# Optimization experiments

Measured on AMD Instinct MI355X. Metric: run time of the kernel, lower is better.

The kernel has to match this reference:

```python
import jax, jax.numpy as jnp
import numpy as np

NUM_HEADS = 8
D_MODEL = 512
HEAD_DIM = D_MODEL // NUM_HEADS
LN_EPS = 1e-5


def setup_inputs() -> dict:
    key = jax.random.key(0)
    ks = jax.random.split(key, 12)
    B, S = 8, 1024
    P = 2 * S - 1  # relative position length
    s = 0.02
    return {
        "x": jax.random.normal(ks[0], (B, S, D_MODEL), jnp.float32),
        "pos_emb": jax.random.normal(ks[1], (P, D_MODEL), jnp.float32),
        "ln_w": jnp.ones((D_MODEL,), jnp.float32),
        "ln_b": jnp.zeros((D_MODEL,), jnp.float32),
        "Wq": jax.random.normal(ks[2], (D_MODEL, D_MODEL), jnp.float32) * s,
        "bq": jax.random.normal(ks[3], (D_MODEL,), jnp.float32) * s,
        "Wk": jax.random.normal(ks[4], (D_MODEL, D_MODEL), jnp.float32) * s,
        "bk": jax.random.normal(ks[5], (D_MODEL,), jnp.float32) * s,
        "Wv": jax.random.normal(ks[6], (D_MODEL, D_MODEL), jnp.float32) * s,
        "bv": jax.random.normal(ks[7], (D_MODEL,), jnp.float32) * s,
        "Wo": jax.random.normal(ks[8], (D_MODEL, D_MODEL), jnp.float32) * s,
        "bo": jax.random.normal(ks[9], (D_MODEL,), jnp.float32) * s,
        "Wp": jax.random.normal(ks[10], (D_MODEL, D_MODEL), jnp.float32) * s,
        "pos_bias_u": jax.random.normal(ks[11], (D_MODEL,), jnp.float32) * s,
        "pos_bias_v": jax.random.normal(jax.random.fold_in(key, 99), (D_MODEL,), jnp.float32) * s,
    }


def _rel_shift(x):
    # x: [B, H, S, P] -> Transformer-XL relative shift, return [B, H, S, S]
    b, h, s, p = x.shape
    x = jnp.pad(x, ((0, 0), (0, 0), (0, 0), (1, 0)))  # pad one zero column on left
    x = x.reshape(b, h, p + 1, s)[:, :, 1:, :]
    x = x.reshape(b, h, s, p)
    return x[:, :, :, :s]


def reference(x, pos_emb, ln_w, ln_b, Wq, bq, Wk, bk, Wv, bv, Wo, bo, Wp,
              pos_bias_u, pos_bias_v):
    B, S, D = x.shape
    H, hd = NUM_HEADS, HEAD_DIM
    # LayerNorm
    mu = jnp.mean(x, axis=-1, keepdims=True)
    var = jnp.mean(jnp.square(x - mu), axis=-1, keepdims=True)
    h_ = (x - mu) * jax.lax.rsqrt(var + LN_EPS) * ln_w + ln_b
    # Projections (torch Linear: y = x @ W.T + b)
    q = (h_ @ Wq.T + bq).reshape(B, S, H, hd).transpose(0, 2, 1, 3)  # [B,H,S,hd]
    k = (h_ @ Wk.T + bk).reshape(B, S, H, hd).transpose(0, 2, 1, 3)
    v = (h_ @ Wv.T + bv).reshape(B, S, H, hd).transpose(0, 2, 1, 3)
    bias_u = pos_bias_u.reshape(1, H, 1, hd)
    bias_v = pos_bias_v.reshape(1, H, 1, hd)
    content = jnp.einsum('bhqd,bhkd->bhqk', q + bias_u, k)
    # Positional projection: [P, D] -> [H, P, hd]
    p = (pos_emb @ Wp.T).reshape(-1, H, hd).transpose(1, 0, 2)
    pos_score = jnp.einsum('bhqd,hpd->bhqp', q + bias_v, p)
    pos_score = _rel_shift(pos_score)
    scale = 1.0 / np.sqrt(hd).astype(np.float32)
    attn = jax.nn.softmax((content + pos_score) * scale, axis=-1)
    out = jnp.einsum('bhqk,bhkd->bhqd', attn, v)
    out = out.transpose(0, 2, 1, 3).reshape(B, S, D)
    out = out @ Wo.T + bo
    return x + out
```

## Files before the change

### kernel.cpp

```cpp
#include <hip/hip_runtime.h>
#include <hip/hip_bf16.h>


typedef __attribute__((ext_vector_type(8))) short  s16x8;
typedef __attribute__((ext_vector_type(8))) __bf16 bfv8;
typedef __attribute__((ext_vector_type(4))) float  f32x4;
typedef __attribute__((ext_vector_type(4))) unsigned u32x4;

__device__ __forceinline__ float b2f(short s){
  unsigned u = ((unsigned)(unsigned short)s) << 16;
  float f; __builtin_memcpy(&f, &u, 4); return f;
}
__device__ __forceinline__ short f2b(float f){
  unsigned u; __builtin_memcpy(&u, &f, 4);
  u = (u + 0x7fffu + ((u >> 16) & 1u)) >> 16;
  return (short)u;
}
__device__ __forceinline__ unsigned pk2(float lo, float hi){
  __hip_bfloat162 t = __float22bfloat162_rn(make_float2(lo, hi));
  unsigned u; __builtin_memcpy(&u, &t, 4); return u;
}
__device__ __forceinline__ f32x4 MFMA(s16x8 a, s16x8 b, f32x4 c){
  return __builtin_amdgcn_mfma_f32_16x16x32_bf16(
      __builtin_bit_cast(bfv8, a), __builtin_bit_cast(bfv8, b), c, 0, 0, 0);
}
__device__ __forceinline__ void gload_lds16(const void* g, void* l){
  __builtin_amdgcn_global_load_lds(
      (const __attribute__((address_space(1))) void*)g,
      (__attribute__((address_space(3))) void*)l, 16, 0, 0);
}
__device__ __forceinline__ void cvt8(const float* in, short* out, size_t i8){
  f32x4 a = *(const f32x4*)(in + i8*8);
  f32x4 b = *(const f32x4*)(in + i8*8 + 4);
  u32x4 o;
  o[0] = pk2(a[0],a[1]); o[1] = pk2(a[2],a[3]);
  o[2] = pk2(b[0],b[1]); o[3] = pk2(b[2],b[3]);
  *(u32x4*)(out + i8*8) = o;
}

__global__ __launch_bounds__(256) void prep_kernel(
    const float* __restrict__ Wq, const float* __restrict__ Wk,
    const float* __restrict__ Wv, const float* __restrict__ Wo,
    const float* __restrict__ Wp, const float* __restrict__ pos,
    const float* __restrict__ x, const float* __restrict__ lnw, const float* __restrict__ lnb,
    short* __restrict__ wqkv, short* __restrict__ wo, short* __restrict__ wp,
    short* __restrict__ posbf, short* __restrict__ h_bf)
{
  int bid = blockIdx.x, tid = threadIdx.x;
  if(bid < 640){
    int w = bid >> 7;
    size_t i = (size_t)(bid & 127)*256 + tid;
    const float* src; short* dst;
    if(w == 0){ src = Wq; dst = wqkv; }
    else if(w == 1){ src = Wk; dst = wqkv + 262144; }
    else if(w == 2){ src = Wv; dst = wqkv + 524288; }
    else if(w == 3){ src = Wo; dst = wo; }
    else { src = Wp; dst = wp; }
    cvt8(src, dst, i);
  } else if(bid < 1152){
    size_t i = (size_t)(bid - 640)*256 + tid;
    if(i < 131008) cvt8(pos, posbf, i);
  } else {
    int row = (bid - 1152)*4 + (tid >> 6);
    int lane = tid & 63;
    const float* xr = x + (size_t)row*512;
    f32x4 v0 = *(const f32x4*)(xr + lane*8);
    f32x4 v1 = *(const f32x4*)(xr + lane*8 + 4);
    float s  = v0[0]+v0[1]+v0[2]+v0[3]+v1[0]+v1[1]+v1[2]+v1[3];
    float s2 = v0[0]*v0[0]+v0[1]*v0[1]+v0[2]*v0[2]+v0[3]*v0[3]
             + v1[0]*v1[0]+v1[1]*v1[1]+v1[2]*v1[2]+v1[3]*v1[3];
    #pragma unroll
    for(int m=1;m<64;m<<=1){ s += __shfl_xor(s,m); s2 += __shfl_xor(s2,m); }
    float mu = s * (1.0f/512.0f);
    float rs = rsqrtf(s2*(1.0f/512.0f) - mu*mu + 1e-5f);
    float y[8];
    #pragma unroll
    for(int e=0;e<8;e++){
      float xv = (e<4)? v0[e] : v1[e-4];
      int d = lane*8 + e;
      y[e] = (xv - mu)*rs*lnw[d] + lnb[d];
    }
    u32x4 o;
    o[0]=pk2(y[0],y[1]); o[1]=pk2(y[2],y[3]); o[2]=pk2(y[4],y[5]); o[3]=pk2(y[6],y[7]);
    *(u32x4*)(h_bf + (size_t)row*512 + lane*8) = o;
  }
}

__global__ __launch_bounds__(256) void gemm_fused(
    const short* __restrict__ h_bf, const short* __restrict__ wqkv,
    const float* __restrict__ bq, const float* __restrict__ bk, const float* __restrict__ bv,
    const short* __restrict__ posbf, const short* __restrict__ wp,
    short* __restrict__ q_sw, short* __restrict__ k_sw, short* __restrict__ v_sw,
    short* __restrict__ p_sw)
{
  __shared__ __align__(16) short smem[9216];
  short* At = smem;
  short* Bt = smem + 4096;
  int bid = blockIdx.x, tid = threadIdx.x;
  int wave = tid >> 6, lane = tid & 63;
  int quad = lane >> 4, l16 = lane & 15;
  int srow = lane >> 2, scol = (lane & 3)*8;
  if(bid < 768){
    int bx = bid % 12, by = bid / 12;
    int m0 = by*128, n0 = bx*128;
    int wm = wave >> 1, wn = wave & 1;
    f32x4 acc[4][4] = {};
    for(int k0=0; k0<512; k0+=32){
      #pragma unroll
      for(int c=0;c<2;c++){
        int rb = (wave + 4*c)*16;
        gload_lds16(h_bf + (size_t)(m0 + rb + srow)*512 + k0 + scol, At + rb*32);
        gload_lds16(wqkv + (size_t)(n0 + rb + srow)*512 + k0 + scol, Bt + rb*32);
      }
      __syncthreads();
      s16x8 af[4], bfr[4];
      #pragma unroll
      for(int i=0;i<4;i++) af[i]  = *(const s16x8*)(At + (wm*64 + i*16 + l16)*32 + quad*8);
      #pragma unroll
      for(int j=0;j<4;j++) bfr[j] = *(const s16x8*)(Bt + (wn*64 + j*16 + l16)*32 + quad*8);
      #pragma unroll
      for(int i=0;i<4;i++)
        #pragma unroll
        for(int j=0;j<4;j++)
          acc[i][j] = MFMA(af[i], bfr[j], acc[i][j]);
      __syncthreads();
    }
    int seg = bx >> 2;
    int nseg = (bx & 3)*128;
    int bb = by >> 3;
    const float* bsrc = (seg==0)? bq : (seg==1)? bk : bv;
    float bias_j[4];
    #pragma unroll
    for(int j=0;j<4;j++) bias_j[j] = bsrc[nseg + wn*64 + j*16 + l16];
    if(seg < 2){
      short* dst = seg ? k_sw : q_sw;
      #pragma unroll
      for(int h2=0; h2<2; h2++){
        if(wm == h2){
          #pragma unroll
          for(int i=0;i<4;i++){
            int lr = i*16 + quad*4;
            #pragma unroll
            for(int j=0;j<4;j++){
              int cl = wn*64 + j*16 + l16;
              unsigned p01 = pk2(acc[i][j][0]+bias_j[j], acc[i][j][1]+bias_j[j]);
              unsigned p23 = pk2(acc[i][j][2]+bias_j[j], acc[i][j][3]+bias_j[j]);
              smem[(lr+0)*136 + cl] = (short)p01;
              smem[(lr+1)*136 + cl] = (short)(p01>>16);
              smem[(lr+2)*136 + cl] = (short)p23;
              smem[(lr+3)*136 + cl] = (short)(p23>>16);
            }
          }
        }
        __syncthreads();
        #pragma unroll
        for(int it=0; it<4; it++){
          int ci = it*4 + wave;
          int hs = ci >> 2, tb = ci & 3;
          s16x8 vv = *(const s16x8*)(smem + (tb*16 + l16)*136 + hs*32 + quad*8);
          int hh = (nseg>>6) + (hs>>1);
          int tg = ((m0 + h2*64)>>4) + tb;
          size_t chunk = ((size_t)((bb*8 + hh)*64 + tg))*2 + (hs&1);
          *(s16x8*)(dst + chunk*512 + (size_t)lane*8) = vv;
        }
        __syncthreads();
      }
    } else {
      #pragma unroll
      for(int h2=0; h2<2; h2++){
        int jt = by*2 + h2;
        if(wm == h2){
          #pragma unroll
          for(int i=0;i<4;i++){
            int tl = i*16 + quad*4;
            #pragma unroll
            for(int j=0;j<4;j++){
              int dl = wn*64 + j*16 + l16;
              unsigned p01 = pk2(acc[i][j][0]+bias_j[j], acc[i][j][1]+bias_j[j]);
              unsigned p23 = pk2(acc[i][j][2]+bias_j[j], acc[i][j][3]+bias_j[j]);
              unsigned* w2 = (unsigned*)(smem + dl*72 + tl);
              w2[0] = p01; w2[1] = p23;
            }
          }
        }
        __syncthreads();
        #pragma unroll
        for(int it=0; it<4; it++){
          int ci = it*4 + wave;
          int hl = ci>>3, ds = (ci>>1)&3, jk = ci&1;
          s16x8 vv = *(const s16x8*)(smem + (hl*64 + ds*16 + l16)*72 + jk*32 + quad*8);
          int hh = (nseg>>6) + hl;
          size_t chunk = (((size_t)((bb*8 + hh)*16 + jt))*4 + ds)*2 + jk;
          *(s16x8*)(v_sw + chunk*512 + (size_t)lane*8) = vv;
        }
        __syncthreads();
      }
    }
  } else {
    int pid = bid - 768;
    int bx = pid % 8, by = pid / 8;
    int m0 = by*64, n0 = bx*64;
    int wm = wave >> 1, wn = wave & 1;
    f32x4 acc[2][2] = {};
    for(int k0=0; k0<512; k0+=32){
      int rb = wave*16;
      int ra = m0 + rb + srow; if(ra > 2046) ra = 2046;
      gload_lds16(posbf + (size_t)ra*512 + k0 + scol, At + rb*32);
      gload_lds16(wp + (size_t)(n0 + rb + srow)*512 + k0 + scol, Bt + rb*32);
      __syncthreads();
      s16x8 af[2], bfr[2];
      #pragma unroll
      for(int i=0;i<2;i++) af[i]  = *(const s16x8*)(At + (wm*32 + i*16 + l16)*32 + quad*8);
      #pragma unroll
      for(int j=0;j<2;j++) bfr[j] = *(const s16x8*)(Bt + (wn*32 + j*16 + l16)*32 + quad*8);
      #pragma unroll
      for(int i=0;i<2;i++)
        #pragma unroll
        for(int j=0;j<2;j++)
          acc[i][j] = MFMA(af[i], bfr[j], acc[i][j]);
      __syncthreads();
    }
    #pragma unroll
    for(int i=0;i<2;i++){
      int rowb = m0 + wm*32 + i*16 + quad*4;
      #pragma unroll
      for(int j=0;j<2;j++){
        int col = n0 + wn*32 + j*16 + l16;
        int hh = col>>6, ks = (col>>5)&1, qd = (col>>3)&3, e = col&7;
        int rblk = rowb>>4;
        size_t base = ((size_t)(((hh*128+rblk)*2+ks)*64) + qd*16)*8 + e;
        #pragma unroll
        for(int r=0;r<4;r++)
          p_sw[base + (size_t)(quad*4+r)*8] = f2b(acc[i][j][r]);
      }
    }
  }
}

__global__ __launch_bounds__(256, 3) void attn_kernel(
    const short* __restrict__ q_sw, const short* __restrict__ k_sw,
    const short* __restrict__ v_sw, const short* __restrict__ p_sw,
    const float* __restrict__ bu, const float* __restrict__ bvv,
    short* __restrict__ out)
{
  __shared__ __align__(16) short kv[2][8192];
  __shared__ __align__(16) short pwall[4608];
  int tid = threadIdx.x;
  int wave = tid >> 6, lane = tid & 63, quad = lane >> 4, l16 = lane & 15;
  int h = blockIdx.y, b = blockIdx.z, bh = b*8 + h;
  int iblk = blockIdx.x*4 + wave;
  int iw = iblk*16;
  short* pw = pwall + wave*1152;

  const short* qb = q_sw + (size_t)bh*65536;
  const short* kb = k_sw + (size_t)bh*65536;
  const short* vb = v_sw + (size_t)bh*65536;
  const short* pb = p_sw + (size_t)h*131072;

  s16x8 qu[2], qv[2];
  #pragma unroll
  for(int ks=0;ks<2;ks++){
    s16x8 qr = *(const s16x8*)(qb + ((size_t)(iblk*2+ks)*64 + lane)*8);
    short tu[8], tv[8];
    #pragma unroll
    for(int e=0;e<8;e++){
      int d = h*64 + ks*32 + quad*8 + e;
      float f = b2f(qr[e]);
      tu[e] = f2b((f + bu[d]) * 0.125f);
      tv[e] = f2b((f + bvv[d]) * 0.125f);
    }
    qu[ks] = *(s16x8*)tu; qv[ks] = *(s16x8*)tv;
  }

  s16x8 ones;
  #pragma unroll
  for(int e=0;e<8;e++) ones[e] = (short)0x3F80;

  int srcl[4]; bool lo[4];
  #pragma unroll
  for(int r=0;r<4;r++){
    int il = quad*4 + r;
    srcl[r] = quad*16 + ((l16 + 15 - il) & 15);
    lo[r]   = (l16 <= il);
  }

  f32x4 oacc[4] = {};
  f32x4 lacc = {};
  s16x8 Pa[5][2];

  auto STAGE = [&](int jt, int bufi){
    const short* base = (wave < 2) ? kb : vb;
    #pragma unroll
    for(int r=0;r<4;r++){
      int unit = wave*4 + r;
      gload_lds16(base + (size_t)jt*4096 + (unit&7)*512 + lane*8,
                  &kv[bufi][unit*512]);
    }
  };
  auto LOADPOS = [&](int jt){
    int rb0 = (jt*64 - iw + 1008) >> 4;
    #pragma unroll
    for(int nt=0;nt<5;nt++)
      #pragma unroll
      for(int ks=0;ks<2;ks++)
        Pa[nt][ks] = *(const s16x8*)(pb + (size_t)((rb0+nt)*2+ks)*512 + lane*8);
  };
  auto COMPUTE = [&](const short* Kt, const short* Vt, int next_jt){
    f32x4 ps[5];
    __builtin_amdgcn_s_setprio(1);
    #pragma unroll
    for(int nt=0;nt<5;nt++){
      f32x4 a = {};
      a = MFMA(qv[0], Pa[nt][0], a);
      a = MFMA(qv[1], Pa[nt][1], a);
      ps[nt] = a;
    }
    __builtin_amdgcn_s_setprio(0);
    if(next_jt < 16) LOADPOS(next_jt);
    float rot[4][5];
    #pragma unroll
    for(int r=0;r<4;r++)
      #pragma unroll
      for(int nt=0;nt<5;nt++) rot[r][nt] = __shfl(ps[nt][r], srcl[r]);
    #pragma unroll
    for(int js=0;js<4;js++){
      s16x8 kf0 = *(const s16x8*)(Kt + (js*2+0)*512 + lane*8);
      s16x8 kf1 = *(const s16x8*)(Kt + (js*2+1)*512 + lane*8);
      f32x4 c0;
      #pragma unroll
      for(int r=0;r<4;r++) c0[r] = lo[r] ? rot[r][js] : rot[r][js+1];
      f32x4 a = MFMA(qu[0], kf0, c0);
      a = MFMA(qu[1], kf1, a);
      int col = js*16 + l16;
      unsigned p01 = pk2(__expf(a[0]), __expf(a[1]));
      unsigned p23 = pk2(__expf(a[2]), __expf(a[3]));
      pw[(quad*4+0)*72 + col] = (short)p01;
      pw[(quad*4+1)*72 + col] = (short)(p01>>16);
      pw[(quad*4+2)*72 + col] = (short)p23;
      pw[(quad*4+3)*72 + col] = (short)(p23>>16);
    }
    __builtin_amdgcn_s_setprio(1);
    #pragma unroll
    for(int jk=0;jk<2;jk++){
      s16x8 pa = *(const s16x8*)(pw + l16*72 + jk*32 + quad*8);
      lacc = MFMA(pa, ones, lacc);
      #pragma unroll
      for(int ds=0;ds<4;ds++){
        s16x8 vf = *(const s16x8*)(Vt + (ds*2+jk)*512 + lane*8);
        oacc[ds] = MFMA(pa, vf, oacc[ds]);
      }
    }
    __builtin_amdgcn_s_setprio(0);
  };

  STAGE(0, 0);
  LOADPOS(0);
  __syncthreads();

  #pragma unroll 1
  for(int jt2=0; jt2<8; ++jt2){
    int jt = jt2*2;
    STAGE(jt+1, 1);
    COMPUTE(&kv[0][0], &kv[0][4096], jt+1);
    __syncthreads();
    if(jt2 < 7) STAGE(jt+2, 0);
    COMPUTE(&kv[1][0], &kv[1][4096], jt+2);
    __syncthreads();
  }

  float rl[4];
  #pragma unroll
  for(int r=0;r<4;r++) rl[r] = __builtin_amdgcn_rcpf(lacc[r]);
  #pragma unroll
  for(int ds=0; ds<4; ds++)
    #pragma unroll
    for(int r=0;r<4;r++)
      out[((size_t)(b*1024 + iw + quad*4 + r))*512 + h*64 + ds*16 + l16] =
          f2b(oacc[ds][r] * rl[r]);
}

__global__ __launch_bounds__(256) void gemm_out(
    const short* __restrict__ A, const short* __restrict__ B,
    const float* __restrict__ bias, const float* __restrict__ resid,
    float* __restrict__ Cout)
{
  __shared__ __align__(16) short At[64*32];
  __shared__ __align__(16) short Bt[64*32];
  int tid = threadIdx.x;
  int wave = tid >> 6, lane = tid & 63;
  int quad = lane >> 4, l16 = lane & 15;
  int wm = wave >> 1, wn = wave & 1;
  int m0 = blockIdx.y*64, n0 = blockIdx.x*64;
  int srow = lane >> 2, scol = (lane & 3)*8;
  f32x4 acc[2][2] = {};
  for(int k0=0; k0<512; k0+=32){
    int rb = wave*16;
    gload_lds16(A + (size_t)(m0 + rb + srow)*512 + k0 + scol, At + rb*32);
    gload_lds16(B + (size_t)(n0 + rb + srow)*512 + k0 + scol, Bt + rb*32);
    __syncthreads();
    s16x8 af[2], bfr[2];
    #pragma unroll
    for(int i=0;i<2;i++) af[i]  = *(const s16x8*)(At + (wm*32 + i*16 + l16)*32 + quad*8);
    #pragma unroll
    for(int j=0;j<2;j++) bfr[j] = *(const s16x8*)(Bt + (wn*32 + j*16 + l16)*32 + quad*8);
    #pragma unroll
    for(int i=0;i<2;i++)
      #pragma unroll
      for(int j=0;j<2;j++)
        acc[i][j] = MFMA(af[i], bfr[j], acc[i][j]);
    __syncthreads();
  }
  #pragma unroll
  for(int i=0;i<2;i++){
    int rowb = m0 + wm*32 + i*16 + quad*4;
    #pragma unroll
    for(int j=0;j<2;j++){
      int col = n0 + wn*32 + j*16 + l16;
      float bv = bias[col];
      #pragma unroll
      for(int r=0;r<4;r++){
        size_t idx = (size_t)(rowb + r)*512 + col;
        Cout[idx] = acc[i][j][r] + bv + resid[idx];
      }
    }
  }
}

extern "C" void kernel_launch(void* const* d_in, const int* in_sizes, int n_in,
                              void* d_out, int out_size, void* d_ws, size_t ws_size,
                              hipStream_t stream)
{
  const float* x    = (const float*)d_in[0];
  const float* pos  = (const float*)d_in[1];
  const float* lnw  = (const float*)d_in[2];
  const float* lnb  = (const float*)d_in[3];
  const float* Wq   = (const float*)d_in[4];
  const float* bq   = (const float*)d_in[5];
  const float* Wk   = (const float*)d_in[6];
  const float* bk   = (const float*)d_in[7];
  const float* Wv   = (const float*)d_in[8];
  const float* bv   = (const float*)d_in[9];
  const float* Wo   = (const float*)d_in[10];
  const float* bo   = (const float*)d_in[11];
  const float* Wp   = (const float*)d_in[12];
  const float* pbu  = (const float*)d_in[13];
  const float* pbv  = (const float*)d_in[14];
  float* out = (float*)d_out;

  char* ws = (char*)d_ws;
  short* h_bf    = (short*)(ws);
  short* q_sw    = (short*)(ws + ( 8u<<20));
  short* k_sw    = (short*)(ws + (16u<<20));
  short* v_sw    = (short*)(ws + (24u<<20));
  short* a_bf    = (short*)(ws + (32u<<20));
  short* p_sw    = (short*)(ws + (40u<<20));
  short* pos_bf  = (short*)(ws + (42u<<20));
  short* wqkv_bf = (short*)(ws + (44u<<20));
  short* wo_bf   = (short*)(ws + (47u<<20));
  short* wp_bf   = (short*)(ws + (47u<<20) + (512u<<10));

  prep_kernel<<<dim3(3200), 256, 0, stream>>>(Wq, Wk, Wv, Wo, Wp, pos,
                                              x, lnw, lnb,
                                              wqkv_bf, wo_bf, wp_bf, pos_bf, h_bf);
  gemm_fused<<<dim3(1024), 256, 0, stream>>>(h_bf, wqkv_bf, bq, bk, bv,
                                             pos_bf, wp_bf,
                                             q_sw, k_sw, v_sw, p_sw);
  attn_kernel<<<dim3(16,8,8), 256, 0, stream>>>(q_sw, k_sw, v_sw, p_sw, pbu, pbv, a_bf);
  gemm_out<<<dim3(8,128), 256, 0, stream>>>(a_bf, wo_bf, bo, x, out);
  (void)in_sizes; (void)n_in; (void)out_size; (void)ws_size;
}
```

Measured before the change: 199.0 us.

## Single-buffer V in attention, raise occupancy, remap blocks across XCDs

The attention kernel now double-buffers only K tiles and keeps a single V tile in LDS. V is loaded just-in-time for each tile, and an extra barrier is added before the PV MFMAs. This cuts LDS use so launch bounds can request 4 blocks per CU instead of 3. The grid becomes 1D with a swizzled block index that groups each (batch, head)'s query tiles onto the same XCD for K/V/P cache locality. The cost is two barriers per tile instead of one, and V loads are exposed with less overlap.

```diff
diff --git a/kernel.cpp b/kernel.cpp
--- a/kernel.cpp
+++ b/kernel.cpp
@@ -237,18 +237,22 @@
   }
 }
 
-__global__ __launch_bounds__(256, 3) void attn_kernel(
+__global__ __launch_bounds__(256, 4) void attn_kernel(
     const short* __restrict__ q_sw, const short* __restrict__ k_sw,
     const short* __restrict__ v_sw, const short* __restrict__ p_sw,
     const float* __restrict__ bu, const float* __restrict__ bvv,
     short* __restrict__ out)
 {
-  __shared__ __align__(16) short kv[2][8192];
+  __shared__ __align__(16) short kK[2][4096];
+  __shared__ __align__(16) short vV[4096];
   __shared__ __align__(16) short pwall[4608];
   int tid = threadIdx.x;
   int wave = tid >> 6, lane = tid & 63, quad = lane >> 4, l16 = lane & 15;
-  int h = blockIdx.y, b = blockIdx.z, bh = b*8 + h;
-  int iblk = blockIdx.x*4 + wave;
+  int bid0 = blockIdx.x;
+  int nb = (bid0 & 7)*128 + (bid0 >> 3);
+  int qt = nb & 15, bh = nb >> 4;
+  int h = bh & 7, b = bh >> 3;
+  int iblk = qt*4 + wave;
   int iw = iblk*16;
   short* pw = pwall + wave*1152;
 
@@ -288,13 +292,22 @@
   f32x4 lacc = {};
   s16x8 Pa[5][2];
 
-  auto STAGE = [&](int jt, int bufi){
-    const short* base = (wave < 2) ? kb : vb;
-    #pragma unroll
-    for(int r=0;r<4;r++){
-      int unit = wave*4 + r;
-      gload_lds16(base + (size_t)jt*4096 + (unit&7)*512 + lane*8,
-                  &kv[bufi][unit*512]);
+  auto STAGE_K = [&](int jt, int bufi){
+    if(wave < 2){
+      #pragma unroll
+      for(int r=0;r<4;r++){
+        int u = wave*4 + r;
+        gload_lds16(kb + (size_t)jt*4096 + u*512 + lane*8, &kK[bufi][u*512]);
+      }
+    }
+  };
+  auto STAGE_V = [&](int jt){
+    if(wave >= 2){
+      #pragma unroll
+      for(int r=0;r<4;r++){
+        int u = (wave-2)*4 + r;
+        gload_lds16(vb + (size_t)jt*4096 + u*512 + lane*8, &vV[u*512]);
+      }
     }
   };
   auto LOADPOS = [&](int jt){
@@ -305,7 +318,17 @@
       for(int ks=0;ks<2;ks++)
         Pa[nt][ks] = *(const s16x8*)(pb + (size_t)((rb0+nt)*2+ks)*512 + lane*8);
   };
-  auto COMPUTE = [&](const short* Kt, const short* Vt, int next_jt){
+
+  STAGE_K(0, 0);
+  LOADPOS(0);
+  __syncthreads();
+
+  #pragma unroll 1
+  for(int jt=0; jt<16; ++jt){
+    int cur = jt & 1;
+    STAGE_V(jt);
+    if(jt < 15) STAGE_K(jt+1, cur^1);
+    const short* Kt = &kK[cur][0];
     f32x4 ps[5];
     __builtin_amdgcn_s_setprio(1);
     #pragma unroll
@@ -316,7 +339,7 @@
       ps[nt] = a;
     }
     __builtin_amdgcn_s_setprio(0);
-    if(next_jt < 16) LOADPOS(next_jt);
+    if(jt < 15) LOADPOS(jt+1);
     float rot[4][5];
     #pragma unroll
     for(int r=0;r<4;r++)
@@ -339,6 +362,7 @@
       pw[(quad*4+2)*72 + col] = (short)p23;
       pw[(quad*4+3)*72 + col] = (short)(p23>>16);
     }
+    __syncthreads();
     __builtin_amdgcn_s_setprio(1);
     #pragma unroll
     for(int jk=0;jk<2;jk++){
@@ -346,25 +370,11 @@
       lacc = MFMA(pa, ones, lacc);
       #pragma unroll
       for(int ds=0;ds<4;ds++){
-        s16x8 vf = *(const s16x8*)(Vt + (ds*2+jk)*512 + lane*8);
+        s16x8 vf = *(const s16x8*)(&vV[(ds*2+jk)*512] + lane*8);
         oacc[ds] = MFMA(pa, vf, oacc[ds]);
       }
     }
     __builtin_amdgcn_s_setprio(0);
-  };
-
-  STAGE(0, 0);
-  LOADPOS(0);
-  __syncthreads();
-
-  #pragma unroll 1
-  for(int jt2=0; jt2<8; ++jt2){
-    int jt = jt2*2;
-    STAGE(jt+1, 1);
-    COMPUTE(&kv[0][0], &kv[0][4096], jt+1);
-    __syncthreads();
-    if(jt2 < 7) STAGE(jt+2, 0);
-    COMPUTE(&kv[1][0], &kv[1][4096], jt+2);
     __syncthreads();
   }
 
@@ -465,7 +475,7 @@
   gemm_fused<<<dim3(1024), 256, 0, stream>>>(h_bf, wqkv_bf, bq, bk, bv,
                                              pos_bf, wp_bf,
                                              q_sw, k_sw, v_sw, p_sw);
-  attn_kernel<<<dim3(16,8,8), 256, 0, stream>>>(q_sw, k_sw, v_sw, p_sw, pbu, pbv, a_bf);
+  attn_kernel<<<dim3(1024), 256, 0, stream>>>(q_sw, k_sw, v_sw, p_sw, pbu, pbv, a_bf);
   gemm_out<<<dim3(8,128), 256, 0, stream>>>(a_bf, wo_bf, bo, x, out);
   (void)in_sizes; (void)n_in; (void)out_size; (void)ws_size;
 }
```

Result: slower. 204.3 us (+2.7%).
